# Kernel optimization log

Hardware: AMD Instinct MI355X
Metric: run time of the kernel (lower is better)

Reference implementation:

```python
import jax, jax.numpy as jnp
import numpy as np

EMBED_DIM = 128
NUM_HEADS = 4
HEAD_DIM = EMBED_DIM // NUM_HEADS


def setup_inputs() -> dict:
    key = jax.random.key(0)
    ks = jax.random.split(key, 12)
    B, N, D = 4, 4096, EMBED_DIM
    s = 1.0 / np.sqrt(D)
    inp = {
        "query": jax.random.normal(ks[0], (B, N, D), dtype=jnp.float32),
        "key": jax.random.normal(ks[1], (B, N, D), dtype=jnp.float32),
        "value": jax.random.normal(ks[2], (B, N, D), dtype=jnp.float32),
        "Wq": jax.random.uniform(ks[3], (D, D), jnp.float32, -s, s),
        "bq": jax.random.uniform(ks[4], (D,), jnp.float32, -s, s),
        "Wk": jax.random.uniform(ks[5], (D, D), jnp.float32, -s, s),
        "bk": jax.random.uniform(ks[6], (D,), jnp.float32, -s, s),
        "Wv": jax.random.uniform(ks[7], (D, D), jnp.float32, -s, s),
        "bv": jax.random.uniform(ks[8], (D,), jnp.float32, -s, s),
        "Wo": jax.random.uniform(ks[9], (D, D), jnp.float32, -s, s),
        "bo": jax.random.uniform(ks[10], (D,), jnp.float32, -s, s),
    }
    return inp


def reference(query, key, value, Wq, bq, Wk, bk, Wv, bv, Wo, bo):
    B, N, D = query.shape
    H, Dh = NUM_HEADS, HEAD_DIM
    scale = Dh ** -0.5
    # Linear projections (torch Linear: x @ W.T + b), split heads -> [B, H, N, Dh]
    Q = (query @ Wq.T + bq).reshape(B, N, H, Dh).transpose(0, 2, 1, 3)
    K = (key @ Wk.T + bk).reshape(B, N, H, Dh).transpose(0, 2, 1, 3)
    V = (value @ Wv.T + bv).reshape(B, N, H, Dh).transpose(0, 2, 1, 3)
    # Attention scores [B, H, N, N]
    scores = jnp.einsum('bhqd,bhkd->bhqk', Q, K) * scale
    attn = jax.nn.softmax(scores, axis=-1)
    ctx = jnp.einsum('bhqk,bhkd->bhqd', attn, V)  # [B, H, N, Dh]
    ctx = ctx.transpose(0, 2, 1, 3).reshape(B, N, D)
    return ctx @ Wo.T + bo
```

## Files before the change

kernel.cpp:

```cpp
#include <hip/hip_runtime.h>
#include <hip/hip_bf16.h>

#define N_SEQ 4096
#define DIM   128
#define NH    4
#define DH    32
#define BATCH 4

#define QSCALE 0.25503495870989204f

typedef __bf16 bf16x8 __attribute__((ext_vector_type(8)));
typedef __bf16 bf16x2 __attribute__((ext_vector_type(2)));
typedef __bf16 bf16x4 __attribute__((ext_vector_type(4)));
typedef float  f32x4  __attribute__((ext_vector_type(4)));

#define MFMA(a, b, c) __builtin_amdgcn_mfma_f32_16x16x32_bf16((a), (b), (c), 0, 0, 0)

static __device__ __forceinline__ bf16x8 cvt8(const float* __restrict__ p) {
    const float4* f4 = reinterpret_cast<const float4*>(p);
    float4 a = f4[0], b = f4[1];
    bf16x8 r;
    r[0] = (__bf16)a.x; r[1] = (__bf16)a.y; r[2] = (__bf16)a.z; r[3] = (__bf16)a.w;
    r[4] = (__bf16)b.x; r[5] = (__bf16)b.y; r[6] = (__bf16)b.z; r[7] = (__bf16)b.w;
    return r;
}

__global__ __launch_bounds__(256) void convert_w(
    const float* __restrict__ Wq, const float* __restrict__ Wk,
    const float* __restrict__ Wv, const float* __restrict__ Wo,
    __bf16* __restrict__ Wb)
{
    const int i = (blockIdx.x * 256 + threadIdx.x) * 4;
    const float* srcs[4] = {Wq, Wk, Wv, Wo};
    #pragma unroll
    for (int w = 0; w < 4; w++) {
        float4 v = *reinterpret_cast<const float4*>(srcs[w] + i);
        bf16x4 o = {(__bf16)v.x, (__bf16)v.y, (__bf16)v.z, (__bf16)v.w};
        *reinterpret_cast<bf16x4*>(Wb + w * (DIM * DIM) + i) = o;
    }
}

__global__ __launch_bounds__(256) void proj_qkv(
    const float* __restrict__ xq, const float* __restrict__ xk, const float* __restrict__ xv,
    const __bf16* __restrict__ Wb,
    const float* __restrict__ bq, const float* __restrict__ bk, const float* __restrict__ bv,
    __bf16* __restrict__ Qs, __bf16* __restrict__ Kb, __bf16* __restrict__ Vt)
{
    const int z = blockIdx.z;
    const float* x    = (z == 0) ? xq : ((z == 1) ? xk : xv);
    const float* bias = (z == 0) ? bq : ((z == 1) ? bk : bv);
    const __bf16* W   = Wb + z * (DIM * DIM);
    const int b    = blockIdx.y;
    const int wave = threadIdx.x >> 6;
    const int lane = threadIdx.x & 63;
    const int quad = lane >> 4, l15 = lane & 15;
    const int n0   = blockIdx.x * 64 + wave * 16;

    bf16x8 a[4];
    const float* xrow = x + (b * N_SEQ + n0 + l15) * DIM + quad * 8;
    a[0] = cvt8(xrow);      a[1] = cvt8(xrow + 32);
    a[2] = cvt8(xrow + 64); a[3] = cvt8(xrow + 96);

    for (int t = 0; t < 8; t++) {
        f32x4 acc = {0.f, 0.f, 0.f, 0.f};
        const __bf16* wrow = W + (t * 16 + l15) * DIM + quad * 8;
        bf16x8 w0 = *(const bf16x8*)(wrow);
        bf16x8 w1 = *(const bf16x8*)(wrow + 32);
        bf16x8 w2 = *(const bf16x8*)(wrow + 64);
        bf16x8 w3 = *(const bf16x8*)(wrow + 96);

        if (z != 2) {
            acc = MFMA(a[0], w0, acc);
            acc = MFMA(a[1], w1, acc);
            acc = MFMA(a[2], w2, acc);
            acc = MFMA(a[3], w3, acc);

            const int d  = t * 16 + l15;
            const int h  = d >> 5, dh = d & 31;
            const float bias_v = bias[d];
            if (z == 0) {
                __bf16* dst = Qs + ((b * NH + h) * N_SEQ) * DH + dh;
                #pragma unroll
                for (int r = 0; r < 4; r++) {
                    const int n = n0 + quad * 4 + r;
                    dst[n * DH] = (__bf16)((acc[r] + bias_v) * QSCALE);
                }
            } else {
                __bf16* dst = Kb + ((b * NH + h) * N_SEQ) * DH + dh;
                #pragma unroll
                for (int r = 0; r < 4; r++) {
                    const int n = n0 + quad * 4 + r;
                    const int np = (n & ~63) | (((n & 3) << 4) | ((n & 63) >> 2));
                    dst[np * DH] = (__bf16)(acc[r] + bias_v);
                }
            }
        } else {
            acc = MFMA(w0, a[0], acc);
            acc = MFMA(w1, a[1], acc);
            acc = MFMA(w2, a[2], acc);
            acc = MFMA(w3, a[3], acc);

            const int n = n0 + l15;
            #pragma unroll
            for (int r = 0; r < 4; r++) {
                const int d = t * 16 + quad * 4 + r;
                const int h = d >> 5, dh = d & 31;
                Vt[((b * NH + h) * DH + dh) * N_SEQ + n] = (__bf16)(acc[r] + bias[d]);
            }
        }
    }
}

__global__ __launch_bounds__(256, 4) void flash_attn(
    const __bf16* __restrict__ Qs, const __bf16* __restrict__ Kb,
    const __bf16* __restrict__ Vt, __bf16* __restrict__ ctxb)
{
    __shared__ __align__(16) char smem[28672];
    char* const Kbase = smem;
    char* const Vbase = smem + 10240;
    char* const Pbase = smem + 19456;

    const int bid  = blockIdx.x;
    const int bh   = bid & 15;
    const int qc   = bid >> 4;
    const int tid  = threadIdx.x;
    const int wave = tid >> 6, lane = tid & 63;
    const int quad = lane >> 4, l15 = lane & 15;
    const int n0   = qc * 64 + wave * 16;

    const __bf16* Qp = Qs + (bh * N_SEQ + n0) * DH;
    bf16x8 qf = *(const bf16x8*)(Qp + l15 * DH + quad * 8);

    const __bf16* gK = Kb + (size_t)bh * N_SEQ * DH + tid * 8;
    const __bf16* gV = Vt + ((size_t)bh * DH + (tid >> 3)) * N_SEQ + (tid & 7) * 8;
    const int kofsK = (tid >> 2) * 80 + (tid & 3) * 16;
    const int kofsV = (tid >> 3) * 144 + (tid & 7) * 16;

    {
        bf16x8 kr = *(const bf16x8*)(gK);
        bf16x8 vr = *(const bf16x8*)(gV);
        *(bf16x8*)(Kbase + kofsK) = kr;
        *(bf16x8*)(Vbase + kofsV) = vr;
    }
    __syncthreads();

    f32x4 c0 = {0.f,0.f,0.f,0.f}, c1 = {0.f,0.f,0.f,0.f};
    float l0[4] = {0.f,0.f,0.f,0.f};
    char* const Pw = Pbase + wave * 2304;
    const f32x4 z4 = {0.f,0.f,0.f,0.f};

    for (int kb = 0; kb < N_SEQ / 64; kb++) {
        const int cur = kb & 1;
        const char* Kc = Kbase + cur * 5120;
        const char* Vc = Vbase + cur * 4608;

        const int kn = (kb + 1) & (N_SEQ / 64 - 1);
        bf16x8 krn = *(const bf16x8*)(gK + kn * 64 * DH);
        bf16x8 vrn = *(const bf16x8*)(gV + kn * 64);

        bf16x8 kf0 = *(const bf16x8*)(Kc + l15 * 80 + quad * 16);
        bf16x8 kf1 = *(const bf16x8*)(Kc + (16 + l15) * 80 + quad * 16);
        bf16x8 kf2 = *(const bf16x8*)(Kc + (32 + l15) * 80 + quad * 16);
        bf16x8 kf3 = *(const bf16x8*)(Kc + (48 + l15) * 80 + quad * 16);

        f32x4 s0 = MFMA(qf, kf0, z4), s1 = MFMA(qf, kf1, z4);
        f32x4 s2 = MFMA(qf, kf2, z4), s3 = MFMA(qf, kf3, z4);

        #pragma unroll
        for (int r = 0; r < 4; r++) {
            float p0 = __builtin_amdgcn_exp2f(s0[r]);
            float p1 = __builtin_amdgcn_exp2f(s1[r]);
            float p2 = __builtin_amdgcn_exp2f(s2[r]);
            float p3 = __builtin_amdgcn_exp2f(s3[r]);
            l0[r] += (p0 + p1) + (p2 + p3);
            bf16x4 pk = {(__bf16)p0, (__bf16)p1, (__bf16)p2, (__bf16)p3};
            *(bf16x4*)(Pw + (quad * 4 + r) * 144 + l15 * 8) = pk;
        }

        bf16x8 pf0 = *(const bf16x8*)(Pw + l15 * 144 + quad * 16);
        bf16x8 pf1 = *(const bf16x8*)(Pw + l15 * 144 + 64 + quad * 16);
        bf16x8 vf00 = *(const bf16x8*)(Vc + l15 * 144 + quad * 16);
        bf16x8 vf01 = *(const bf16x8*)(Vc + (16 + l15) * 144 + quad * 16);
        bf16x8 vf10 = *(const bf16x8*)(Vc + l15 * 144 + 64 + quad * 16);
        bf16x8 vf11 = *(const bf16x8*)(Vc + (16 + l15) * 144 + 64 + quad * 16);

        c0 = MFMA(pf0, vf00, c0); c1 = MFMA(pf0, vf01, c1);
        c0 = MFMA(pf1, vf10, c0); c1 = MFMA(pf1, vf11, c1);

        *(bf16x8*)(Kbase + (cur ^ 1) * 5120 + kofsK) = krn;
        *(bf16x8*)(Vbase + (cur ^ 1) * 4608 + kofsV) = vrn;
        __syncthreads();
    }

    const int b = bh >> 2, h = bh & 3;
    #pragma unroll
    for (int r = 0; r < 4; r++) {
        float ls = l0[r];
        ls += __shfl_xor(ls, 1); ls += __shfl_xor(ls, 2);
        ls += __shfl_xor(ls, 4); ls += __shfl_xor(ls, 8);
        const float inv = 1.0f / ls;
        const int n = n0 + quad * 4 + r;
        __bf16* dst = ctxb + (b * N_SEQ + n) * DIM + h * DH;
        dst[l15]      = (__bf16)(c0[r] * inv);
        dst[16 + l15] = (__bf16)(c1[r] * inv);
    }
}

__global__ __launch_bounds__(256) void out_proj(
    const __bf16* __restrict__ ctxb, const __bf16* __restrict__ WoB,
    const float* __restrict__ bo, float* __restrict__ out)
{
    const int b    = blockIdx.y;
    const int wave = threadIdx.x >> 6, lane = threadIdx.x & 63;
    const int quad = lane >> 4, l15 = lane & 15;
    const int n0   = blockIdx.x * 64 + wave * 16;

    bf16x8 a[4];
    const __bf16* crow = ctxb + (b * N_SEQ + n0 + l15) * DIM + quad * 8;
    a[0] = *(const bf16x8*)(crow);
    a[1] = *(const bf16x8*)(crow + 32);
    a[2] = *(const bf16x8*)(crow + 64);
    a[3] = *(const bf16x8*)(crow + 96);

    for (int t = 0; t < 8; t++) {
        f32x4 acc = {0.f, 0.f, 0.f, 0.f};
        const __bf16* wrow = WoB + (t * 16 + l15) * DIM + quad * 8;
        acc = MFMA(a[0], *(const bf16x8*)(wrow),      acc);
        acc = MFMA(a[1], *(const bf16x8*)(wrow + 32), acc);
        acc = MFMA(a[2], *(const bf16x8*)(wrow + 64), acc);
        acc = MFMA(a[3], *(const bf16x8*)(wrow + 96), acc);

        const int d = t * 16 + l15;
        const float bias_v = bo[d];
        #pragma unroll
        for (int r = 0; r < 4; r++) {
            const int n = n0 + quad * 4 + r;
            out[(b * N_SEQ + n) * DIM + d] = acc[r] + bias_v;
        }
    }
}

extern "C" void kernel_launch(void* const* d_in, const int* in_sizes, int n_in,
                              void* d_out, int out_size, void* d_ws, size_t ws_size,
                              hipStream_t stream)
{
    const float* query = (const float*)d_in[0];
    const float* key   = (const float*)d_in[1];
    const float* value = (const float*)d_in[2];
    const float* Wq = (const float*)d_in[3];
    const float* bq = (const float*)d_in[4];
    const float* Wk = (const float*)d_in[5];
    const float* bk = (const float*)d_in[6];
    const float* Wv = (const float*)d_in[7];
    const float* bv = (const float*)d_in[8];
    const float* Wo = (const float*)d_in[9];
    const float* bo = (const float*)d_in[10];
    float* out = (float*)d_out;

    char* ws = (char*)d_ws;
    const size_t e = (size_t)BATCH * N_SEQ * DIM;
    __bf16* Qs   = (__bf16*)(ws);
    __bf16* Kb   = (__bf16*)(ws + 2 * e);
    __bf16* Vt   = (__bf16*)(ws + 4 * e);
    __bf16* ctxb = (__bf16*)(ws + 6 * e);
    __bf16* Wb   = (__bf16*)(ws + 8 * e);

    convert_w<<<dim3(16), 256, 0, stream>>>(Wq, Wk, Wv, Wo, Wb);
    proj_qkv<<<dim3(64, BATCH, 3), 256, 0, stream>>>(
        query, key, value, Wb, bq, bk, bv, Qs, Kb, Vt);
    flash_attn<<<dim3(1024), 256, 0, stream>>>(Qs, Kb, Vt, ctxb);
    out_proj<<<dim3(64, BATCH), 256, 0, stream>>>(ctxb, Wb + 3 * DIM * DIM, bo, out);
}
```

Measured before the change: 181.8 us.

## Double query rows per wave, keep P in registers, fuse weight conversion

Flash attention now gives each wave 32 query rows instead of 16, reusing every K/V fragment loaded from LDS across two query tiles. It also swaps MFMA operand order so the exp'd scores land directly in the register layout needed for the PV product, which removes the LDS round-trip for P. Weight conversion to bf16 moves into the projection kernels through LDS, dropping the separate convert_w launch. Projection and output stores are vectorised, and V is written in a permuted order to match. The cost is more registers per wave (launch bound lowered to 2) and half as many attention blocks (512 instead of 1024).

```diff
diff --git a/kernel.cpp b/kernel.cpp
--- a/kernel.cpp
+++ b/kernel.cpp
@@ -25,100 +25,86 @@
     return r;
 }
 
-__global__ __launch_bounds__(256) void convert_w(
-    const float* __restrict__ Wq, const float* __restrict__ Wk,
-    const float* __restrict__ Wv, const float* __restrict__ Wo,
-    __bf16* __restrict__ Wb)
-{
-    const int i = (blockIdx.x * 256 + threadIdx.x) * 4;
-    const float* srcs[4] = {Wq, Wk, Wv, Wo};
-    #pragma unroll
-    for (int w = 0; w < 4; w++) {
-        float4 v = *reinterpret_cast<const float4*>(srcs[w] + i);
-        bf16x4 o = {(__bf16)v.x, (__bf16)v.y, (__bf16)v.z, (__bf16)v.w};
-        *reinterpret_cast<bf16x4*>(Wb + w * (DIM * DIM) + i) = o;
-    }
-}
-
 __global__ __launch_bounds__(256) void proj_qkv(
     const float* __restrict__ xq, const float* __restrict__ xk, const float* __restrict__ xv,
-    const __bf16* __restrict__ Wb,
+    const float* __restrict__ Wq, const float* __restrict__ Wk, const float* __restrict__ Wv,
     const float* __restrict__ bq, const float* __restrict__ bk, const float* __restrict__ bv,
     __bf16* __restrict__ Qs, __bf16* __restrict__ Kb, __bf16* __restrict__ Vt)
 {
+    __shared__ __align__(16) char wlds[34816];
     const int z = blockIdx.z;
     const float* x    = (z == 0) ? xq : ((z == 1) ? xk : xv);
+    const float* Wf   = (z == 0) ? Wq : ((z == 1) ? Wk : Wv);
     const float* bias = (z == 0) ? bq : ((z == 1) ? bk : bv);
-    const __bf16* W   = Wb + z * (DIM * DIM);
     const int b    = blockIdx.y;
-    const int wave = threadIdx.x >> 6;
-    const int lane = threadIdx.x & 63;
+    const int tid  = threadIdx.x;
+    const int wave = tid >> 6, lane = tid & 63;
     const int quad = lane >> 4, l15 = lane & 15;
     const int n0   = blockIdx.x * 64 + wave * 16;
+
+    {
+        const int r = tid >> 1, half = tid & 1;
+        const float* wsrc = Wf + r * DIM + half * 64;
+        char* wdst = wlds + r * 272 + half * 128;
+        #pragma unroll
+        for (int i = 0; i < 8; i++)
+            *(bf16x8*)(wdst + i * 16) = cvt8(wsrc + i * 8);
+    }
 
     bf16x8 a[4];
     const float* xrow = x + (b * N_SEQ + n0 + l15) * DIM + quad * 8;
     a[0] = cvt8(xrow);      a[1] = cvt8(xrow + 32);
     a[2] = cvt8(xrow + 64); a[3] = cvt8(xrow + 96);
-
+    __syncthreads();
+
+    const int n = n0 + l15;
     for (int t = 0; t < 8; t++) {
+        const char* wr = wlds + (t * 16 + l15) * 272 + quad * 16;
+        bf16x8 w0 = *(const bf16x8*)(wr);
+        bf16x8 w1 = *(const bf16x8*)(wr + 64);
+        bf16x8 w2 = *(const bf16x8*)(wr + 128);
+        bf16x8 w3 = *(const bf16x8*)(wr + 192);
+
         f32x4 acc = {0.f, 0.f, 0.f, 0.f};
-        const __bf16* wrow = W + (t * 16 + l15) * DIM + quad * 8;
-        bf16x8 w0 = *(const bf16x8*)(wrow);
-        bf16x8 w1 = *(const bf16x8*)(wrow + 32);
-        bf16x8 w2 = *(const bf16x8*)(wrow + 64);
-        bf16x8 w3 = *(const bf16x8*)(wrow + 96);
-
-        if (z != 2) {
-            acc = MFMA(a[0], w0, acc);
-            acc = MFMA(a[1], w1, acc);
-            acc = MFMA(a[2], w2, acc);
-            acc = MFMA(a[3], w3, acc);
-
-            const int d  = t * 16 + l15;
-            const int h  = d >> 5, dh = d & 31;
-            const float bias_v = bias[d];
-            if (z == 0) {
-                __bf16* dst = Qs + ((b * NH + h) * N_SEQ) * DH + dh;
-                #pragma unroll
-                for (int r = 0; r < 4; r++) {
-                    const int n = n0 + quad * 4 + r;
-                    dst[n * DH] = (__bf16)((acc[r] + bias_v) * QSCALE);
-                }
-            } else {
-                __bf16* dst = Kb + ((b * NH + h) * N_SEQ) * DH + dh;
-                #pragma unroll
-                for (int r = 0; r < 4; r++) {
-                    const int n = n0 + quad * 4 + r;
-                    const int np = (n & ~63) | (((n & 3) << 4) | ((n & 63) >> 2));
-                    dst[np * DH] = (__bf16)(acc[r] + bias_v);
-                }
-            }
+        acc = MFMA(w0, a[0], acc);
+        acc = MFMA(w1, a[1], acc);
+        acc = MFMA(w2, a[2], acc);
+        acc = MFMA(w3, a[3], acc);
+
+        const int d0 = t * 16 + quad * 4;
+        if (z == 0) {
+            const int h = d0 >> 5, dh0 = d0 & 31;
+            bf16x4 q4;
+            #pragma unroll
+            for (int r = 0; r < 4; r++)
+                q4[r] = (__bf16)((acc[r] + bias[d0 + r]) * QSCALE);
+            *(bf16x4*)(Qs + ((b * NH + h) * N_SEQ + n) * DH + dh0) = q4;
+        } else if (z == 1) {
+            const int h = d0 >> 5, dh0 = d0 & 31;
+            bf16x4 k4;
+            #pragma unroll
+            for (int r = 0; r < 4; r++)
+                k4[r] = (__bf16)(acc[r] + bias[d0 + r]);
+            *(bf16x4*)(Kb + ((b * NH + h) * N_SEQ + n) * DH + dh0) = k4;
         } else {
-            acc = MFMA(w0, a[0], acc);
-            acc = MFMA(w1, a[1], acc);
-            acc = MFMA(w2, a[2], acc);
-            acc = MFMA(w3, a[3], acc);
-
-            const int n = n0 + l15;
+            const int nl = n & 63;
+            const int np = (n & ~63) | (nl & 35) | ((nl & 12) << 1) | ((nl & 16) >> 2);
             #pragma unroll
             for (int r = 0; r < 4; r++) {
-                const int d = t * 16 + quad * 4 + r;
-                const int h = d >> 5, dh = d & 31;
-                Vt[((b * NH + h) * DH + dh) * N_SEQ + n] = (__bf16)(acc[r] + bias[d]);
+                const int d = d0 + r, h = d >> 5, dh = d & 31;
+                Vt[((b * NH + h) * DH + dh) * N_SEQ + np] = (__bf16)(acc[r] + bias[d]);
             }
         }
     }
 }
 
-__global__ __launch_bounds__(256, 4) void flash_attn(
+__global__ __launch_bounds__(256, 2) void flash_attn(
     const __bf16* __restrict__ Qs, const __bf16* __restrict__ Kb,
     const __bf16* __restrict__ Vt, __bf16* __restrict__ ctxb)
 {
-    __shared__ __align__(16) char smem[28672];
+    __shared__ __align__(16) char smem[19456];
     char* const Kbase = smem;
     char* const Vbase = smem + 10240;
-    char* const Pbase = smem + 19456;
 
     const int bid  = blockIdx.x;
     const int bh   = bid & 15;
@@ -126,10 +112,11 @@
     const int tid  = threadIdx.x;
     const int wave = tid >> 6, lane = tid & 63;
     const int quad = lane >> 4, l15 = lane & 15;
-    const int n0   = qc * 64 + wave * 16;
+    const int n0   = qc * 128 + wave * 32;
 
     const __bf16* Qp = Qs + (bh * N_SEQ + n0) * DH;
-    bf16x8 qf = *(const bf16x8*)(Qp + l15 * DH + quad * 8);
+    bf16x8 qf0 = *(const bf16x8*)(Qp + l15 * DH + quad * 8);
+    bf16x8 qf1 = *(const bf16x8*)(Qp + (16 + l15) * DH + quad * 8);
 
     const __bf16* gK = Kb + (size_t)bh * N_SEQ * DH + tid * 8;
     const __bf16* gV = Vt + ((size_t)bh * DH + (tid >> 3)) * N_SEQ + (tid & 7) * 8;
@@ -144,9 +131,9 @@
     }
     __syncthreads();
 
-    f32x4 c0 = {0.f,0.f,0.f,0.f}, c1 = {0.f,0.f,0.f,0.f};
-    float l0[4] = {0.f,0.f,0.f,0.f};
-    char* const Pw = Pbase + wave * 2304;
+    f32x4 c00 = {0.f,0.f,0.f,0.f}, c01 = {0.f,0.f,0.f,0.f};
+    f32x4 c10 = {0.f,0.f,0.f,0.f}, c11 = {0.f,0.f,0.f,0.f};
+    float l0 = 0.f, l1 = 0.f;
     const f32x4 z4 = {0.f,0.f,0.f,0.f};
 
     for (int kb = 0; kb < N_SEQ / 64; kb++) {
@@ -163,57 +150,88 @@
         bf16x8 kf2 = *(const bf16x8*)(Kc + (32 + l15) * 80 + quad * 16);
         bf16x8 kf3 = *(const bf16x8*)(Kc + (48 + l15) * 80 + quad * 16);
 
-        f32x4 s0 = MFMA(qf, kf0, z4), s1 = MFMA(qf, kf1, z4);
-        f32x4 s2 = MFMA(qf, kf2, z4), s3 = MFMA(qf, kf3, z4);
-
+        f32x4 s00 = MFMA(kf0, qf0, z4), s10 = MFMA(kf1, qf0, z4);
+        f32x4 s20 = MFMA(kf2, qf0, z4), s30 = MFMA(kf3, qf0, z4);
+        f32x4 s01 = MFMA(kf0, qf1, z4), s11 = MFMA(kf1, qf1, z4);
+        f32x4 s21 = MFMA(kf2, qf1, z4), s31 = MFMA(kf3, qf1, z4);
+
+        bf16x8 pf00, pf10, pf01, pf11;
         #pragma unroll
         for (int r = 0; r < 4; r++) {
-            float p0 = __builtin_amdgcn_exp2f(s0[r]);
-            float p1 = __builtin_amdgcn_exp2f(s1[r]);
-            float p2 = __builtin_amdgcn_exp2f(s2[r]);
-            float p3 = __builtin_amdgcn_exp2f(s3[r]);
-            l0[r] += (p0 + p1) + (p2 + p3);
-            bf16x4 pk = {(__bf16)p0, (__bf16)p1, (__bf16)p2, (__bf16)p3};
-            *(bf16x4*)(Pw + (quad * 4 + r) * 144 + l15 * 8) = pk;
-        }
-
-        bf16x8 pf0 = *(const bf16x8*)(Pw + l15 * 144 + quad * 16);
-        bf16x8 pf1 = *(const bf16x8*)(Pw + l15 * 144 + 64 + quad * 16);
+            float p0 = __builtin_amdgcn_exp2f(s00[r]);
+            float p1 = __builtin_amdgcn_exp2f(s10[r]);
+            float p2 = __builtin_amdgcn_exp2f(s20[r]);
+            float p3 = __builtin_amdgcn_exp2f(s30[r]);
+            l0 += (p0 + p1) + (p2 + p3);
+            pf00[r] = (__bf16)p0; pf00[4 + r] = (__bf16)p1;
+            pf10[r] = (__bf16)p2; pf10[4 + r] = (__bf16)p3;
+        }
+        #pragma unroll
+        for (int r = 0; r < 4; r++) {
+            float p0 = __builtin_amdgcn_exp2f(s01[r]);
+            float p1 = __builtin_amdgcn_exp2f(s11[r]);
+            float p2 = __builtin_amdgcn_exp2f(s21[r]);
+            float p3 = __builtin_amdgcn_exp2f(s31[r]);
+            l1 += (p0 + p1) + (p2 + p3);
+            pf01[r] = (__bf16)p0; pf01[4 + r] = (__bf16)p1;
+            pf11[r] = (__bf16)p2; pf11[4 + r] = (__bf16)p3;
+        }
+
         bf16x8 vf00 = *(const bf16x8*)(Vc + l15 * 144 + quad * 16);
-        bf16x8 vf01 = *(const bf16x8*)(Vc + (16 + l15) * 144 + quad * 16);
-        bf16x8 vf10 = *(const bf16x8*)(Vc + l15 * 144 + 64 + quad * 16);
+        bf16x8 vf10 = *(const bf16x8*)(Vc + (16 + l15) * 144 + quad * 16);
+        bf16x8 vf01 = *(const bf16x8*)(Vc + l15 * 144 + 64 + quad * 16);
         bf16x8 vf11 = *(const bf16x8*)(Vc + (16 + l15) * 144 + 64 + quad * 16);
 
-        c0 = MFMA(pf0, vf00, c0); c1 = MFMA(pf0, vf01, c1);
-        c0 = MFMA(pf1, vf10, c0); c1 = MFMA(pf1, vf11, c1);
+        c00 = MFMA(vf00, pf00, c00); c01 = MFMA(vf10, pf00, c01);
+        c00 = MFMA(vf01, pf10, c00); c01 = MFMA(vf11, pf10, c01);
+        c10 = MFMA(vf00, pf01, c10); c11 = MFMA(vf10, pf01, c11);
+        c10 = MFMA(vf01, pf11, c10); c11 = MFMA(vf11, pf11, c11);
 
         *(bf16x8*)(Kbase + (cur ^ 1) * 5120 + kofsK) = krn;
         *(bf16x8*)(Vbase + (cur ^ 1) * 4608 + kofsV) = vrn;
         __syncthreads();
     }
 
+    l0 += __shfl_xor(l0, 16); l0 += __shfl_xor(l0, 32);
+    l1 += __shfl_xor(l1, 16); l1 += __shfl_xor(l1, 32);
+    const float inv0 = 1.0f / l0, inv1 = 1.0f / l1;
+
     const int b = bh >> 2, h = bh & 3;
     #pragma unroll
-    for (int r = 0; r < 4; r++) {
-        float ls = l0[r];
-        ls += __shfl_xor(ls, 1); ls += __shfl_xor(ls, 2);
-        ls += __shfl_xor(ls, 4); ls += __shfl_xor(ls, 8);
-        const float inv = 1.0f / ls;
-        const int n = n0 + quad * 4 + r;
-        __bf16* dst = ctxb + (b * N_SEQ + n) * DIM + h * DH;
-        dst[l15]      = (__bf16)(c0[r] * inv);
-        dst[16 + l15] = (__bf16)(c1[r] * inv);
+    for (int qt = 0; qt < 2; qt++) {
+        const float inv = qt ? inv1 : inv0;
+        const int q = n0 + qt * 16 + l15;
+        #pragma unroll
+        for (int dt = 0; dt < 2; dt++) {
+            f32x4 cc = qt ? (dt ? c11 : c10) : (dt ? c01 : c00);
+            __bf16* dst = ctxb + ((size_t)(b * N_SEQ + q)) * DIM + h * DH + dt * 16 + quad * 4;
+            bf16x2 e0 = {(__bf16)(cc[0] * inv), (__bf16)(cc[1] * inv)};
+            bf16x2 e1 = {(__bf16)(cc[2] * inv), (__bf16)(cc[3] * inv)};
+            *(bf16x2*)(dst)     = e0;
+            *(bf16x2*)(dst + 2) = e1;
+        }
     }
 }
 
 __global__ __launch_bounds__(256) void out_proj(
-    const __bf16* __restrict__ ctxb, const __bf16* __restrict__ WoB,
+    const __bf16* __restrict__ ctxb, const float* __restrict__ Wo,
     const float* __restrict__ bo, float* __restrict__ out)
 {
+    __shared__ __align__(16) char wlds[34816];
     const int b    = blockIdx.y;
-    const int wave = threadIdx.x >> 6, lane = threadIdx.x & 63;
+    const int tid  = threadIdx.x;
+    const int wave = tid >> 6, lane = tid & 63;
     const int quad = lane >> 4, l15 = lane & 15;
     const int n0   = blockIdx.x * 64 + wave * 16;
+
+    {
+        const int r = tid >> 1, half = tid & 1;
+        const float* wsrc = Wo + r * DIM + half * 64;
+        char* wdst = wlds + r * 272 + half * 128;
+        #pragma unroll
+        for (int i = 0; i < 8; i++)
+            *(bf16x8*)(wdst + i * 16) = cvt8(wsrc + i * 8);
+    }
 
     bf16x8 a[4];
     const __bf16* crow = ctxb + (b * N_SEQ + n0 + l15) * DIM + quad * 8;
@@ -221,22 +239,29 @@
     a[1] = *(const bf16x8*)(crow + 32);
     a[2] = *(const bf16x8*)(crow + 64);
     a[3] = *(const bf16x8*)(crow + 96);
-
+    __syncthreads();
+
+    const int n = n0 + l15;
     for (int t = 0; t < 8; t++) {
+        const char* wr = wlds + (t * 16 + l15) * 272 + quad * 16;
+        bf16x8 w0 = *(const bf16x8*)(wr);
+        bf16x8 w1 = *(const bf16x8*)(wr + 64);
+        bf16x8 w2 = *(const bf16x8*)(wr + 128);
+        bf16x8 w3 = *(const bf16x8*)(wr + 192);
+
         f32x4 acc = {0.f, 0.f, 0.f, 0.f};
-        const __bf16* wrow = WoB + (t * 16 + l15) * DIM + quad * 8;
-        acc = MFMA(a[0], *(const bf16x8*)(wrow),      acc);
-        acc = MFMA(a[1], *(const bf16x8*)(wrow + 32), acc);
-        acc = MFMA(a[2], *(const bf16x8*)(wrow + 64), acc);
-        acc = MFMA(a[3], *(const bf16x8*)(wrow + 96), acc);
-
-        const int d = t * 16 + l15;
-        const float bias_v = bo[d];
-        #pragma unroll
-        for (int r = 0; r < 4; r++) {
-            const int n = n0 + quad * 4 + r;
-            out[(b * N_SEQ + n) * DIM + d] = acc[r] + bias_v;
-        }
+        acc = MFMA(w0, a[0], acc);
+        acc = MFMA(w1, a[1], acc);
+        acc = MFMA(w2, a[2], acc);
+        acc = MFMA(w3, a[3], acc);
+
+        const int d0 = t * 16 + quad * 4;
+        float4 o;
+        o.x = acc[0] + bo[d0];
+        o.y = acc[1] + bo[d0 + 1];
+        o.z = acc[2] + bo[d0 + 2];
+        o.w = acc[3] + bo[d0 + 3];
+        *(float4*)(out + (b * N_SEQ + n) * DIM + d0) = o;
     }
 }
 
@@ -263,11 +288,9 @@
     __bf16* Kb   = (__bf16*)(ws + 2 * e);
     __bf16* Vt   = (__bf16*)(ws + 4 * e);
     __bf16* ctxb = (__bf16*)(ws + 6 * e);
-    __bf16* Wb   = (__bf16*)(ws + 8 * e);
-
-    convert_w<<<dim3(16), 256, 0, stream>>>(Wq, Wk, Wv, Wo, Wb);
+
     proj_qkv<<<dim3(64, BATCH, 3), 256, 0, stream>>>(
-        query, key, value, Wb, bq, bk, bv, Qs, Kb, Vt);
-    flash_attn<<<dim3(1024), 256, 0, stream>>>(Qs, Kb, Vt, ctxb);
-    out_proj<<<dim3(64, BATCH), 256, 0, stream>>>(ctxb, Wb + 3 * DIM * DIM, bo, out);
-}
+        query, key, value, Wq, Wk, Wv, bq, bk, bv, Qs, Kb, Vt);
+    flash_attn<<<dim3(512), 256, 0, stream>>>(Qs, Kb, Vt, ctxb);
+    out_proj<<<dim3(64, BATCH), 256, 0, stream>>>(ctxb, Wo, bo, out);
+}
```

After: 151.9 us. 16.5% less time.
